# Optimization experiments

Hardware: AMD Instinct MI355X
Metric: run time of the kernel (lower is better)

Reference implementation:

```python
import math
import jax, jax.numpy as jnp
import numpy as np


def fht(x):
    """Normalized fast Hadamard transform over the last axis (size = power of 2)."""
    n = x.shape[-1]
    pre = x.shape[:-1]
    y = x.reshape(-1, n)
    h = 1
    while h < n:
        y = y.reshape(-1, n // (2 * h), 2, h)
        a = y[:, :, 0, :]
        b = y[:, :, 1, :]
        y = jnp.stack([a + b, a - b], axis=2)
        h *= 2
    return y.reshape(*pre, n) * jnp.float32(1.0 / math.sqrt(n))


def setup_inputs() -> dict:
    key = jax.random.key(0)
    ks = jax.random.split(key, 8)
    B, N, M, G = 8192, 4096, 4096, 512  # tokens, in_features(n_pad), out_features(m_pad), n_pad//8
    CB = 256  # E8 shell codebook entries (8-bit indices), each an 8-dim lattice point
    x = jax.random.normal(ks[0], (B, N), dtype=jnp.float32)
    Qidxs = jax.random.randint(ks[1], (M, G), 0, CB, dtype=jnp.int32)
    Qidxs2 = jax.random.randint(ks[2], (M, G), 0, CB, dtype=jnp.int32)
    SU = jax.random.rademacher(ks[3], (M,), dtype=jnp.float32)  # row sign vector
    SV = jax.random.rademacher(ks[4], (N,), dtype=jnp.float32)  # column sign vector
    codebook = jax.random.normal(ks[5], (CB, 8), dtype=jnp.float32)
    codebook2 = jax.random.normal(ks[6], (CB, 8), dtype=jnp.float32)
    Wscale = jnp.asarray(0.85, dtype=jnp.float32)
    inv_resid_scale = jnp.asarray(0.07, dtype=jnp.float32)  # nonzero -> stage-2 enabled
    return {"x": x, "Qidxs": Qidxs, "Qidxs2": Qidxs2, "SU": SU, "SV": SV,
            "codebook": codebook, "codebook2": codebook2,
            "Wscale": Wscale, "inv_resid_scale": inv_resid_scale}


def reference(x, Qidxs, Qidxs2, SU, SV, codebook, codebook2, Wscale, inv_resid_scale):
    # in_features == n_pad and out_features == m_pad here (powers of 2), so no pad/slice.
    m_pad, g = Qidxs.shape
    n_pad = g * 8
    # 1) input RHT: signs then Hadamard
    x_rht = fht(x * SV[None, :])  # (B, n_pad)
    # 2) dequantize weights in RHT domain: codebook lookup per 8-dim group + residual stage
    W_rht = codebook[Qidxs].reshape(m_pad, n_pad)
    W_rht = W_rht + codebook2[Qidxs2].reshape(m_pad, n_pad) * inv_resid_scale
    # 3) matmul in RHT domain with global scale
    y_rht = (x_rht @ W_rht.T) * Wscale  # (B, m_pad)
    # 4) output inverse RHT: Hadamard then signs
    y = fht(y_rht) * SU[None, :]
    return y
```

## Files before the change

kernel.cpp:

```cpp
#include <hip/hip_runtime.h>

#define B_DIM 8192
#define N_DIM 4096
#define M_DIM 4096
#define G_DIM 512

typedef short bf16x8 __attribute__((ext_vector_type(8)));
typedef float f32x4 __attribute__((ext_vector_type(4)));

typedef __attribute__((address_space(1))) const void gvoid_t;
typedef __attribute__((address_space(3))) void lvoid_t;

__device__ __forceinline__ void load_lds16(const void* g, void* l) {
    __builtin_amdgcn_global_load_lds((gvoid_t*)g, (lvoid_t*)l, 16, 0, 0);
}

__device__ __forceinline__ unsigned lds_u32(const void* p) {
    return (unsigned)(unsigned long long)(lvoid_t*)p;
}

__device__ __forceinline__ unsigned short f2bf(float f) {
    union { float f; unsigned int u; } v; v.f = f;
    unsigned int u = v.u;
    unsigned int r = (u + 0x7fffu + ((u >> 16) & 1u)) >> 16;
    return (unsigned short)r;
}
__device__ __forceinline__ float bf2f(unsigned short s) {
    union { unsigned int u; float f; } v; v.u = ((unsigned int)s) << 16;
    return v.f;
}

__device__ __forceinline__ void h16(float* v) {
#pragma unroll
    for (int h = 1; h < 16; h <<= 1) {
#pragma unroll
        for (int i = 0; i < 16; i++) {
            if (!(i & h)) {
                float a = v[i], b = v[i | h];
                v[i] = a + b;
                v[i | h] = a - b;
            }
        }
    }
}

__device__ __forceinline__ void h64(float* v) {
#pragma unroll
    for (int h = 1; h < 64; h <<= 1) {
#pragma unroll
        for (int i = 0; i < 64; i++) {
            if (!(i & h)) {
                float a = v[i], b = v[i | h];
                v[i] = a + b;
                v[i | h] = a - b;
            }
        }
    }
}

__global__ __launch_bounds__(256) void k_build_w(
    const int* __restrict__ q1, const int* __restrict__ q2,
    const float* __restrict__ cb1, const float* __restrict__ cb2,
    const float* __restrict__ wsp, const float* __restrict__ irsp,
    unsigned short* __restrict__ W) {
    __shared__ float c1[256 * 9];
    __shared__ float c2[256 * 9];
    int t = threadIdx.x;
#pragma unroll
    for (int j = 0; j < 8; j++) {
        c1[t * 9 + j] = cb1[t * 8 + j];
        c2[t * 9 + j] = cb2[t * 8 + j];
    }
    __syncthreads();
    float ws = wsp[0];
    float irs = irsp[0] * ws;
    int gid = blockIdx.x * 256 + t;
    int i1 = q1[gid] * 9;
    int i2 = q2[gid] * 9;
    union { unsigned short s[8]; int4 v; } o;
#pragma unroll
    for (int j = 0; j < 8; j++) {
        o.s[j] = f2bf(c1[i1 + j] * ws + c2[i2 + j] * irs);
    }
    *(int4*)(W + (size_t)gid * 8) = o.v;
}

__global__ __launch_bounds__(256) void k_hadw(
    unsigned short* __restrict__ W, int base_mul, int step, float scale) {
    int c = blockIdx.x * 256 + threadIdx.x;
    int base = blockIdx.y * base_mul;
    float v[64];
#pragma unroll
    for (int j = 0; j < 64; j++)
        v[j] = bf2f(W[(size_t)(base + j * step) * N_DIM + c]);
    h64(v);
#pragma unroll
    for (int j = 0; j < 64; j++)
        W[(size_t)(base + j * step) * N_DIM + c] = f2bf(v[j] * scale);
}

__global__ __launch_bounds__(256) void k_rht_in(
    const float* __restrict__ x, const float* __restrict__ SV,
    unsigned short* __restrict__ out) {
    __shared__ float lds[4352];
    int row = blockIdx.x;
    int t = threadIdx.x;
    const float* xr = x + (size_t)row * N_DIM;
    float v[16];
#pragma unroll
    for (int r = 0; r < 16; r++) {
        int n = t + (r << 8);
        v[r] = xr[n] * SV[n] * 0.015625f;
    }
    h16(v);
#pragma unroll
    for (int r = 0; r < 16; r++) { int n = t + (r << 8); lds[n + (n >> 4)] = v[r]; }
    __syncthreads();
#pragma unroll
    for (int r = 0; r < 16; r++) { int n = (t << 4) + r; v[r] = lds[n + (n >> 4)]; }
    h16(v);
#pragma unroll
    for (int r = 0; r < 16; r++) { int n = (t << 4) + r; lds[n + (n >> 4)] = v[r]; }
    __syncthreads();
#pragma unroll
    for (int r = 0; r < 16; r++) {
        int n = (t & 15) | (r << 4) | ((t >> 4) << 8);
        v[r] = lds[n + (n >> 4)];
    }
    h16(v);
#pragma unroll
    for (int r = 0; r < 16; r++) {
        int n = (t & 15) | (r << 4) | ((t >> 4) << 8);
        lds[n + (n >> 4)] = v[r];
    }
    __syncthreads();
    unsigned short* orow = out + (size_t)row * N_DIM;
#pragma unroll
    for (int r = 0; r < 16; r++) {
        int n = t + (r << 8);
        orow[n] = f2bf(lds[n + (n >> 4)]);
    }
}

#define DSR(D, A, OFF) \
    asm volatile("ds_read_b128 %0, %1 offset:" #OFF : "=v"(D) : "v"(A))

__global__ __launch_bounds__(512, 2) void k_gemm(
    const unsigned short* __restrict__ A,
    const unsigned short* __restrict__ Bw,
    const float* __restrict__ SU,
    float* __restrict__ C) {
    __shared__ __align__(16) unsigned short lds[4 * 16384];

    int t = threadIdx.x;
    int w = t >> 6;
    int l = t & 63;

    int lin = blockIdx.x;
    int xcd = lin & 7;
    int idx = lin >> 3;
    int bn = xcd * 2 + (idx >> 5);
    int bm = idx & 31;

    int lx = l ^ (l >> 3);
    const unsigned short* aS0 =
        A + (size_t)(bm * 256 + w * 16 + (lx >> 2)) * N_DIM + (lx & 3) * 8;
    const unsigned short* aS1 = aS0 + (size_t)128 * N_DIM;
    const unsigned short* bS0 =
        Bw + (size_t)(bn * 256 + w * 16 + (lx >> 2)) * N_DIM + (lx & 3) * 8;
    const unsigned short* bS1 = bS0 + (size_t)128 * N_DIM;

    int wm = w >> 2;
    int wn = w & 3;
    int quad = l >> 4;
    int ln = l & 15;
    unsigned ldsU = lds_u32(lds);
    unsigned aBase = ldsU +
        (unsigned)(((((wm * 128) + ln) << 6) | (quad << 4)) ^ ((ln >> 1) << 4));
    unsigned bBase = ldsU + 16384u +
        (unsigned)(((((wn * 64) + ln) << 6) | (quad << 4)) ^ ((ln >> 1) << 4));

    f32x4 acc[8][4];
#pragma unroll
    for (int i = 0; i < 8; i++)
#pragma unroll
        for (int j = 0; j < 4; j++) {
            f32x4 z = {0.f, 0.f, 0.f, 0.f};
            acc[i][j] = z;
        }

#define STAGE(KT) do {                                              \
        int kt_ = (KT);                                             \
        int ks_ = kt_ < 127 ? kt_ : 127;                            \
        unsigned short* d_ = lds + ((unsigned)kt_ & 3u) * 16384 + w * 512; \
        const unsigned short* sa0_ = aS0 + ks_ * 32;                \
        const unsigned short* sa1_ = aS1 + ks_ * 32;                \
        const unsigned short* sb0_ = bS0 + ks_ * 32;                \
        const unsigned short* sb1_ = bS1 + ks_ * 32;                \
        load_lds16(sa0_, d_);                                       \
        load_lds16(sa1_, d_ + 4096);                                \
        load_lds16(sb0_, d_ + 8192);                                \
        load_lds16(sb1_, d_ + 12288);                               \
    } while (0)

    STAGE(0);
    STAGE(1);
    STAGE(2);

    for (int k = 0; k < N_DIM / 32; k++) {
        asm volatile("s_waitcnt vmcnt(8)");
        __builtin_amdgcn_s_barrier();
        STAGE(k + 3);

        unsigned au = aBase + (unsigned)(k & 3) * 32768u;
        unsigned bu = bBase + (unsigned)(k & 3) * 32768u;
        bf16x8 af[8], bfr[4];
        DSR(af[0], au, 0);
        DSR(af[1], au, 1024);
        DSR(af[2], au, 2048);
        DSR(af[3], au, 3072);
        DSR(af[4], au, 4096);
        DSR(af[5], au, 5120);
        DSR(af[6], au, 6144);
        DSR(af[7], au, 7168);
        DSR(bfr[0], bu, 0);
        DSR(bfr[1], bu, 1024);
        DSR(bfr[2], bu, 2048);
        DSR(bfr[3], bu, 3072);
        asm volatile("s_waitcnt lgkmcnt(0)");
        __builtin_amdgcn_sched_barrier(0);

        __builtin_amdgcn_s_setprio(1);
#pragma unroll
        for (int i = 0; i < 8; i++)
#pragma unroll
            for (int j = 0; j < 4; j++)
                acc[i][j] = __builtin_amdgcn_mfma_f32_16x16x32_bf16(
                    af[i], bfr[j], acc[i][j], 0, 0, 0);
        __builtin_amdgcn_s_setprio(0);
    }
    asm volatile("s_waitcnt vmcnt(0)");

#pragma unroll
    for (int j = 0; j < 4; j++) {
        int col = bn * 256 + wn * 64 + j * 16 + ln;
        float su = SU[col];
#pragma unroll
        for (int i = 0; i < 8; i++) {
#pragma unroll
            for (int r = 0; r < 4; r++) {
                int rowg = bm * 256 + wm * 128 + i * 16 + quad * 4 + r;
                C[(size_t)rowg * M_DIM + col] = acc[i][j][r] * su;
            }
        }
    }
#undef STAGE
}

extern "C" void kernel_launch(void* const* d_in, const int* in_sizes, int n_in,
                              void* d_out, int out_size, void* d_ws, size_t ws_size,
                              hipStream_t stream) {
    const float* x    = (const float*)d_in[0];
    const int*   q1   = (const int*)d_in[1];
    const int*   q2   = (const int*)d_in[2];
    const float* SU   = (const float*)d_in[3];
    const float* SV   = (const float*)d_in[4];
    const float* cb1  = (const float*)d_in[5];
    const float* cb2  = (const float*)d_in[6];
    const float* wsp  = (const float*)d_in[7];
    const float* irsp = (const float*)d_in[8];
    float* out = (float*)d_out;

    unsigned short* xrht = (unsigned short*)d_ws;
    unsigned short* Wb   = xrht + (size_t)B_DIM * N_DIM;

    k_build_w<<<dim3((M_DIM * G_DIM) / 256), dim3(256), 0, stream>>>(
        q1, q2, cb1, cb2, wsp, irsp, Wb);
    k_hadw<<<dim3(N_DIM / 256, 64), dim3(256), 0, stream>>>(Wb, 1, 64, 1.0f);
    k_hadw<<<dim3(N_DIM / 256, 64), dim3(256), 0, stream>>>(Wb, 64, 1, 0.015625f);
    k_rht_in<<<dim3(B_DIM), dim3(256), 0, stream>>>(x, SV, xrht);
    k_gemm<<<dim3(512), dim3(512), 0, stream>>>(xrht, Wb, SU, out);
}
```

Before: 516.3 us.

## Vectorize input RHT with 64-thread blocks and restructure GEMM loop barriers

The input Hadamard kernel drops from 256 to 64 threads per row. Each thread now does float4 loads and 16-byte bf16 stores and runs four 16-point transforms per stage. In the GEMM, the hand-written ds_read_b128 inline asm and the setprio calls are replaced with plain C++ LDS vector loads. The wait and barrier move from the top to the bottom of each k-iteration, so the compiler is free to interleave LDS reads with the MFMAs. Risks include weaker control over instruction scheduling in the GEMM and lower occupancy or parallelism in the RHT kernel.

```diff
diff --git a/kernel.cpp b/kernel.cpp
--- a/kernel.cpp
+++ b/kernel.cpp
@@ -13,10 +13,6 @@
 
 __device__ __forceinline__ void load_lds16(const void* g, void* l) {
     __builtin_amdgcn_global_load_lds((gvoid_t*)g, (lvoid_t*)l, 16, 0, 0);
-}
-
-__device__ __forceinline__ unsigned lds_u32(const void* p) {
-    return (unsigned)(unsigned long long)(lvoid_t*)p;
 }
 
 __device__ __forceinline__ unsigned short f2bf(float f) {
@@ -99,51 +95,70 @@
         W[(size_t)(base + j * step) * N_DIM + c] = f2bf(v[j] * scale);
 }
 
-__global__ __launch_bounds__(256) void k_rht_in(
+__global__ __launch_bounds__(64) void k_rht_in(
     const float* __restrict__ x, const float* __restrict__ SV,
     unsigned short* __restrict__ out) {
     __shared__ float lds[4352];
+    int u = threadIdx.x;
     int row = blockIdx.x;
-    int t = threadIdx.x;
     const float* xr = x + (size_t)row * N_DIM;
-    float v[16];
+    float v[4][16];
 #pragma unroll
     for (int r = 0; r < 16; r++) {
-        int n = t + (r << 8);
-        v[r] = xr[n] * SV[n] * 0.015625f;
-    }
-    h16(v);
-#pragma unroll
-    for (int r = 0; r < 16; r++) { int n = t + (r << 8); lds[n + (n >> 4)] = v[r]; }
-    __syncthreads();
-#pragma unroll
-    for (int r = 0; r < 16; r++) { int n = (t << 4) + r; v[r] = lds[n + (n >> 4)]; }
-    h16(v);
-#pragma unroll
-    for (int r = 0; r < 16; r++) { int n = (t << 4) + r; lds[n + (n >> 4)] = v[r]; }
-    __syncthreads();
+        int n = 4 * u + (r << 8);
+        float4 a = *(const float4*)(xr + n);
+        float4 s = *(const float4*)(SV + n);
+        v[0][r] = a.x * s.x * 0.015625f;
+        v[1][r] = a.y * s.y * 0.015625f;
+        v[2][r] = a.z * s.z * 0.015625f;
+        v[3][r] = a.w * s.w * 0.015625f;
+    }
+#pragma unroll
+    for (int i = 0; i < 4; i++) h16(v[i]);
 #pragma unroll
     for (int r = 0; r < 16; r++) {
-        int n = (t & 15) | (r << 4) | ((t >> 4) << 8);
-        v[r] = lds[n + (n >> 4)];
-    }
-    h16(v);
-#pragma unroll
-    for (int r = 0; r < 16; r++) {
-        int n = (t & 15) | (r << 4) | ((t >> 4) << 8);
-        lds[n + (n >> 4)] = v[r];
+#pragma unroll
+        for (int i = 0; i < 4; i++) {
+            int n = (r << 8) + 4 * u + i;
+            lds[n + (n >> 4)] = v[i][r];
+        }
+    }
+    __syncthreads();
+#pragma unroll
+    for (int j = 0; j < 4; j++) {
+        int base = 17 * (u + (j << 6));
+        float w[16];
+#pragma unroll
+        for (int n0 = 0; n0 < 16; n0++) w[n0] = lds[base + n0];
+        h16(w);
+#pragma unroll
+        for (int n0 = 0; n0 < 16; n0++) lds[base + n0] = w[n0];
+    }
+    __syncthreads();
+#pragma unroll
+    for (int j = 0; j < 4; j++) {
+        int base = 272 * ((u >> 4) + (j << 2)) + (u & 15);
+        float w[16];
+#pragma unroll
+        for (int r = 0; r < 16; r++) w[r] = lds[base + 17 * r];
+        h16(w);
+#pragma unroll
+        for (int r = 0; r < 16; r++) lds[base + 17 * r] = w[r];
     }
     __syncthreads();
     unsigned short* orow = out + (size_t)row * N_DIM;
 #pragma unroll
-    for (int r = 0; r < 16; r++) {
-        int n = t + (r << 8);
-        orow[n] = f2bf(lds[n + (n >> 4)]);
-    }
-}
-
-#define DSR(D, A, OFF) \
-    asm volatile("ds_read_b128 %0, %1 offset:" #OFF : "=v"(D) : "v"(A))
+    for (int s = 0; s < 8; s++) {
+        int n = 8 * u + (s << 9);
+        union { unsigned short h[8]; int4 q; } o;
+#pragma unroll
+        for (int jj = 0; jj < 8; jj++) {
+            int nn = n + jj;
+            o.h[jj] = f2bf(lds[nn + (nn >> 4)]);
+        }
+        *(int4*)(orow + n) = o.q;
+    }
+}
 
 __global__ __launch_bounds__(512, 2) void k_gemm(
     const unsigned short* __restrict__ A,
@@ -174,11 +189,10 @@
     int wn = w & 3;
     int quad = l >> 4;
     int ln = l & 15;
-    unsigned ldsU = lds_u32(lds);
-    unsigned aBase = ldsU +
-        (unsigned)(((((wm * 128) + ln) << 6) | (quad << 4)) ^ ((ln >> 1) << 4));
-    unsigned bBase = ldsU + 16384u +
-        (unsigned)(((((wn * 64) + ln) << 6) | (quad << 4)) ^ ((ln >> 1) << 4));
+    unsigned aOff =
+        (unsigned)((((wm * 128 + ln) << 6) | (quad << 4)) ^ ((ln >> 1) << 4)) >> 1;
+    unsigned bOff = 8192u +
+        ((unsigned)((((wn * 64 + ln) << 6) | (quad << 4)) ^ ((ln >> 1) << 4)) >> 1);
 
     f32x4 acc[8][4];
 #pragma unroll
@@ -193,51 +207,40 @@
         int kt_ = (KT);                                             \
         int ks_ = kt_ < 127 ? kt_ : 127;                            \
         unsigned short* d_ = lds + ((unsigned)kt_ & 3u) * 16384 + w * 512; \
-        const unsigned short* sa0_ = aS0 + ks_ * 32;                \
-        const unsigned short* sa1_ = aS1 + ks_ * 32;                \
-        const unsigned short* sb0_ = bS0 + ks_ * 32;                \
-        const unsigned short* sb1_ = bS1 + ks_ * 32;                \
-        load_lds16(sa0_, d_);                                       \
-        load_lds16(sa1_, d_ + 4096);                                \
-        load_lds16(sb0_, d_ + 8192);                                \
-        load_lds16(sb1_, d_ + 12288);                               \
+        load_lds16(aS0 + ks_ * 32, d_);                             \
+        load_lds16(aS1 + ks_ * 32, d_ + 4096);                      \
+        load_lds16(bS0 + ks_ * 32, d_ + 8192);                      \
+        load_lds16(bS1 + ks_ * 32, d_ + 12288);                     \
     } while (0)
 
     STAGE(0);
     STAGE(1);
     STAGE(2);
+    asm volatile("s_waitcnt vmcnt(8)");
+    __builtin_amdgcn_s_barrier();
+    asm volatile("" ::: "memory");
 
     for (int k = 0; k < N_DIM / 32; k++) {
-        asm volatile("s_waitcnt vmcnt(8)");
-        __builtin_amdgcn_s_barrier();
         STAGE(k + 3);
 
-        unsigned au = aBase + (unsigned)(k & 3) * 32768u;
-        unsigned bu = bBase + (unsigned)(k & 3) * 32768u;
+        const unsigned short* aP = lds + ((unsigned)k & 3u) * 16384u + aOff;
+        const unsigned short* bP = lds + ((unsigned)k & 3u) * 16384u + bOff;
         bf16x8 af[8], bfr[4];
-        DSR(af[0], au, 0);
-        DSR(af[1], au, 1024);
-        DSR(af[2], au, 2048);
-        DSR(af[3], au, 3072);
-        DSR(af[4], au, 4096);
-        DSR(af[5], au, 5120);
-        DSR(af[6], au, 6144);
-        DSR(af[7], au, 7168);
-        DSR(bfr[0], bu, 0);
-        DSR(bfr[1], bu, 1024);
-        DSR(bfr[2], bu, 2048);
-        DSR(bfr[3], bu, 3072);
-        asm volatile("s_waitcnt lgkmcnt(0)");
-        __builtin_amdgcn_sched_barrier(0);
-
-        __builtin_amdgcn_s_setprio(1);
+#pragma unroll
+        for (int j = 0; j < 4; j++) bfr[j] = *(const bf16x8*)(bP + j * 512);
+#pragma unroll
+        for (int i = 0; i < 8; i++) af[i] = *(const bf16x8*)(aP + i * 512);
 #pragma unroll
         for (int i = 0; i < 8; i++)
 #pragma unroll
             for (int j = 0; j < 4; j++)
                 acc[i][j] = __builtin_amdgcn_mfma_f32_16x16x32_bf16(
                     af[i], bfr[j], acc[i][j], 0, 0, 0);
-        __builtin_amdgcn_s_setprio(0);
+
+        asm volatile("s_waitcnt lgkmcnt(0)" ::: "memory");
+        asm volatile("s_waitcnt vmcnt(8)");
+        __builtin_amdgcn_s_barrier();
+        asm volatile("" ::: "memory");
     }
     asm volatile("s_waitcnt vmcnt(0)");
 
@@ -278,6 +281,6 @@
         q1, q2, cb1, cb2, wsp, irsp, Wb);
     k_hadw<<<dim3(N_DIM / 256, 64), dim3(256), 0, stream>>>(Wb, 1, 64, 1.0f);
     k_hadw<<<dim3(N_DIM / 256, 64), dim3(256), 0, stream>>>(Wb, 64, 1, 0.015625f);
-    k_rht_in<<<dim3(B_DIM), dim3(256), 0, stream>>>(x, SV, xrht);
+    k_rht_in<<<dim3(B_DIM), dim3(64), 0, stream>>>(x, SV, xrht);
     k_gemm<<<dim3(512), dim3(512), 0, stream>>>(xrht, Wb, SU, out);
 }
```

After: 534.2 us. 1.03x slower.
